# Kernel optimization log

Hardware: AMD Instinct MI355X
Metric: run time of the kernel (lower is better)

## Reference

```python
import jax, jax.numpy as jnp
import numpy as np

RNN_HID = 256
WINDOW = 128
SEQ_LEN = 8192
BATCH = 32
NEG_INF = -1e9


def setup_inputs() -> dict:
    key = jax.random.key(0)
    k1, k2, k3, k4, k5 = jax.random.split(key, 5)
    h_t = jax.random.normal(k1, (BATCH, RNN_HID), dtype=jnp.float32)
    encoder_outputs = jax.random.normal(k2, (BATCH, SEQ_LEN, RNN_HID), dtype=jnp.float32)
    # learned parameters (torch nn.Linear default init approximated with scaled normals)
    W_p = jax.random.normal(k3, (RNN_HID, RNN_HID), dtype=jnp.float32) / jnp.sqrt(RNN_HID)
    v_p = jax.random.normal(k4, (RNN_HID,), dtype=jnp.float32)
    w_att = jax.random.normal(k5, (RNN_HID,), dtype=jnp.float32) / jnp.sqrt(RNN_HID)
    return {"h_t": h_t, "encoder_outputs": encoder_outputs, "W_p": W_p, "v_p": v_p, "w_att": w_att}


def reference(h_t, encoder_outputs, W_p, v_p, w_att):
    B, S, H = encoder_outputs.shape
    # predicted center position p_t per sample
    tanh_out = jnp.tanh(h_t @ W_p.T)                      # [B, H]
    p_t = SEQ_LEN * jax.nn.sigmoid(tanh_out @ v_p)        # [B]
    p_t = jnp.clip(jnp.round(p_t).astype(jnp.int32), 0, SEQ_LEN - 1)
    start = jnp.maximum(p_t - WINDOW, 0)                  # [B]
    end = jnp.minimum(p_t + WINDOW, SEQ_LEN)              # [B]
    rng = jnp.arange(S)[None, :]                          # [1, S]
    mask = (rng >= start[:, None]) & (rng < end[:, None])  # [B, S]
    # scores on masked (zeroed) encoder outputs, then masked softmax
    local = encoder_outputs * mask[:, :, None].astype(encoder_outputs.dtype)
    scores = jnp.einsum('bsh,h->bs', local, w_att)        # [B, S]
    scores = jnp.where(mask, scores, NEG_INF)
    attn_weights = jax.nn.softmax(scores, axis=-1)        # [B, S]
    context_vector = jnp.einsum('bs,bsh->bh', attn_weights, encoder_outputs)
    return context_vector, attn_weights
```

## Files before the change

### kernel.cpp

```cpp
#include <hip/hip_runtime.h>
#include <math.h>

#define BATCH   32
#define SEQ     8192
#define HID     256
#define WIN     128
#define NSLICE  8
#define SLROWS  32

#define WS_PT_OFF   0
#define WS_EXP_OFF  1024
#define WS_SUM_OFF  33792
#define WS_CTX_OFF  34816

__global__ __launch_bounds__(256) void k1_pt_partials(
    const float* __restrict__ h_t,
    const float* __restrict__ W_p,
    const float* __restrict__ v_p,
    float* __restrict__ attn_out,
    double* __restrict__ ws_pt)
{
    const int blk = blockIdx.x;
    const int b   = blk >> 2;
    const int q   = blk & 3;
    const int tid = threadIdx.x;

    __shared__ float  hs[HID];
    __shared__ double part[256];
    __shared__ double redv[64];

    hs[tid] = h_t[b * HID + tid];

    {
        float4* az = (float4*)attn_out + (size_t)blk * 512;
        float4 z = make_float4(0.f, 0.f, 0.f, 0.f);
        az[tid]       = z;
        az[tid + 256] = z;
    }
    __syncthreads();

    const int jl = tid >> 2;
    const int j  = q * 64 + jl;
    const int p4 = tid & 3;
    const float4* wrow = (const float4*)(W_p + (size_t)j * HID + p4 * 64);
    const float*  h4   = &hs[p4 * 64];
    double acc = 0.0;
#pragma unroll
    for (int k = 0; k < 16; ++k) {
        float4 w = wrow[k];
        acc += (double)w.x * h4[k*4+0] + (double)w.y * h4[k*4+1]
             + (double)w.z * h4[k*4+2] + (double)w.w * h4[k*4+3];
    }
    part[tid] = acc;
    __syncthreads();

    if (p4 == 0) {
        double s = part[tid] + part[tid+1] + part[tid+2] + part[tid+3];
        float  t = tanhf((float)s);
        redv[jl] = (double)t * (double)v_p[j];
    }
    __syncthreads();
    for (int off = 32; off > 0; off >>= 1) {
        if (tid < off) redv[tid] += redv[tid + off];
        __syncthreads();
    }
    if (tid == 0) ws_pt[b * 4 + q] = redv[0];
}

__device__ __forceinline__ void window_from_partials(const double* ws_pt, int b,
                                                     int* start, int* end) {
    double x = ws_pt[b*4+0] + ws_pt[b*4+1] + ws_pt[b*4+2] + ws_pt[b*4+3];
    float xf = (float)x;
    float sg = 1.0f / (1.0f + expf(-xf));
    float p  = (float)SEQ * sg;
    int pr = (int)rintf(p);
    pr = min(max(pr, 0), SEQ - 1);
    *start = max(pr - WIN, 0);
    *end   = min(pr + WIN, SEQ);
}

__global__ __launch_bounds__(256) void k2_scores_ctx(
    const float* __restrict__ enc,
    const float* __restrict__ w_att,
    const double* __restrict__ ws_pt,
    float* __restrict__ ws_exp,
    float* __restrict__ ws_sum,
    float* __restrict__ ws_ctx)
{
    const int blk = blockIdx.x;
    const int b   = blk >> 3;
    const int s   = blk & 7;
    const int tid = threadIdx.x;

    __shared__ float wa[HID];
    __shared__ float partial[256];
    __shared__ float es[SLROWS];
    __shared__ int   win_s[2];

    wa[tid] = w_att[tid];
    if (tid == 0) {
        int st, en;
        window_from_partials(ws_pt, b, &st, &en);
        win_s[0] = st; win_s[1] = en;
    }
    __syncthreads();

    const int start = win_s[0];
    const int end   = win_s[1];
    const int g0    = start + s * SLROWS;

    {
        const int r   = tid >> 3;
        const int seg = tid & 7;
        const int g   = g0 + r;
        const int gc  = (g < end) ? g : start;
        const float4* rowp = (const float4*)(enc + ((size_t)b * SEQ + gc) * HID + seg * 32);
        const float*  w4   = &wa[seg * 32];
        float sc = 0.f;
#pragma unroll
        for (int k = 0; k < 8; ++k) {
            float4 e = rowp[k];
            sc += e.x * w4[k*4+0] + e.y * w4[k*4+1] + e.z * w4[k*4+2] + e.w * w4[k*4+3];
        }
        partial[tid] = sc;
    }
    __syncthreads();

    if (tid < SLROWS) {
        const int base = tid * 8;
        float scr = 0.f;
#pragma unroll
        for (int k = 0; k < 8; ++k) scr += partial[base + k];
        const int g = g0 + tid;
        float ev = (g < end) ? expf(scr) : 0.f;
        es[tid] = ev;
        ws_exp[b * 256 + s * SLROWS + tid] = ev;
    }
    __syncthreads();

    if (tid == 0) {
        float sm = 0.f;
#pragma unroll
        for (int k = 0; k < SLROWS; ++k) sm += es[k];
        ws_sum[b * NSLICE + s] = sm;
    }

    {
        float acc = 0.f;
        if (g0 + SLROWS - 1 < end) {
            const float* basep = enc + ((size_t)b * SEQ + g0) * HID + tid;
#pragma unroll
            for (int i = 0; i < SLROWS; ++i)
                acc += es[i] * basep[(size_t)i * HID];
        } else {
#pragma unroll
            for (int i = 0; i < SLROWS; ++i) {
                int g  = g0 + i;
                int gc = (g < end) ? g : start;
                acc += es[i] * enc[((size_t)b * SEQ + gc) * HID + tid];
            }
        }
        ws_ctx[((size_t)b * NSLICE + s) * HID + tid] = acc;
    }
}

__global__ __launch_bounds__(256) void k3_finalize(
    const double* __restrict__ ws_pt,
    const float* __restrict__ ws_exp,
    const float* __restrict__ ws_sum,
    const float* __restrict__ ws_ctx,
    float* __restrict__ ctx_out,
    float* __restrict__ attn_out)
{
    const int b   = blockIdx.x;
    const int tid = threadIdx.x;

    __shared__ int   win_s[2];
    __shared__ float inv_s;

    if (tid == 0) {
        int st, en;
        window_from_partials(ws_pt, b, &st, &en);
        win_s[0] = st; win_s[1] = en;
        float dsum = 0.f;
#pragma unroll
        for (int k = 0; k < NSLICE; ++k) dsum += ws_sum[b * NSLICE + k];
        inv_s = 1.0f / dsum;
    }
    __syncthreads();

    const int start = win_s[0];
    const int L     = win_s[1] - win_s[0];
    const float inv = inv_s;

    float acc = 0.f;
#pragma unroll
    for (int s = 0; s < NSLICE; ++s)
        acc += ws_ctx[((size_t)b * NSLICE + s) * HID + tid];
    ctx_out[b * HID + tid] = acc * inv;

    if (tid < L)
        attn_out[(size_t)b * SEQ + start + tid] = ws_exp[b * 256 + tid] * inv;
}

extern "C" void kernel_launch(void* const* d_in, const int* in_sizes, int n_in,
                              void* d_out, int out_size, void* d_ws, size_t ws_size,
                              hipStream_t stream) {
    const float* h_t   = (const float*)d_in[0];
    const float* enc   = (const float*)d_in[1];
    const float* W_p   = (const float*)d_in[2];
    const float* v_p   = (const float*)d_in[3];
    const float* w_att = (const float*)d_in[4];

    float* ctx_out  = (float*)d_out;
    float* attn_out = (float*)d_out + BATCH * HID;

    char* ws = (char*)d_ws;
    double* ws_pt  = (double*)(ws + WS_PT_OFF);
    float*  ws_exp = (float*)(ws + WS_EXP_OFF);
    float*  ws_sum = (float*)(ws + WS_SUM_OFF);
    float*  ws_ctx = (float*)(ws + WS_CTX_OFF);

    k1_pt_partials<<<BATCH * 4, 256, 0, stream>>>(h_t, W_p, v_p, attn_out, ws_pt);
    k2_scores_ctx<<<BATCH * NSLICE, 256, 0, stream>>>(enc, w_att, ws_pt, ws_exp, ws_sum, ws_ctx);
    k3_finalize<<<BATCH, 256, 0, stream>>>(ws_pt, ws_exp, ws_sum, ws_ctx, ctx_out, attn_out);
}
```

Measured before the change: 15.88 us.

## Fuse position prediction, scoring and finalize into one kernel with last-block reduction

Merges the three kernels into a single launch. Each slice block recomputes the full W_p matvec, tanh and v_p reduction for its batch row to get the window. The last block to finish for each batch, detected with an atomic counter and thread fences, then performs the final normalisation and writes the outputs. This removes two kernel launches and their inter-kernel gaps, but adds an 8x redundant 256x256 fp64 matvec per batch row with poorly coalesced row-per-thread reads of W_p, plus a memset to reset the counters.

After: 49.05 us. 3.09x slower.

```diff
diff --git a/kernel.cpp b/kernel.cpp
--- a/kernel.cpp
+++ b/kernel.cpp
@@ -5,103 +5,77 @@
 #define SEQ     8192
 #define HID     256
 #define WIN     128
-#define NSLICE  8
+#define NSL     8
 #define SLROWS  32
 
-#define WS_PT_OFF   0
-#define WS_EXP_OFF  1024
-#define WS_SUM_OFF  33792
+#define WS_EXP_OFF  0
+#define WS_SUM_OFF  32768
+#define WS_CNT_OFF  33792
 #define WS_CTX_OFF  34816
 
-__global__ __launch_bounds__(256) void k1_pt_partials(
+__global__ __launch_bounds__(256) void fused_local_attn(
     const float* __restrict__ h_t,
+    const float* __restrict__ enc,
     const float* __restrict__ W_p,
     const float* __restrict__ v_p,
+    const float* __restrict__ w_att,
+    float* __restrict__ ctx_out,
     float* __restrict__ attn_out,
-    double* __restrict__ ws_pt)
-{
-    const int blk = blockIdx.x;
-    const int b   = blk >> 2;
-    const int q   = blk & 3;
-    const int tid = threadIdx.x;
-
-    __shared__ float  hs[HID];
-    __shared__ double part[256];
-    __shared__ double redv[64];
-
-    hs[tid] = h_t[b * HID + tid];
-
-    {
-        float4* az = (float4*)attn_out + (size_t)blk * 512;
-        float4 z = make_float4(0.f, 0.f, 0.f, 0.f);
-        az[tid]       = z;
-        az[tid + 256] = z;
-    }
-    __syncthreads();
-
-    const int jl = tid >> 2;
-    const int j  = q * 64 + jl;
-    const int p4 = tid & 3;
-    const float4* wrow = (const float4*)(W_p + (size_t)j * HID + p4 * 64);
-    const float*  h4   = &hs[p4 * 64];
-    double acc = 0.0;
-#pragma unroll
-    for (int k = 0; k < 16; ++k) {
-        float4 w = wrow[k];
-        acc += (double)w.x * h4[k*4+0] + (double)w.y * h4[k*4+1]
-             + (double)w.z * h4[k*4+2] + (double)w.w * h4[k*4+3];
-    }
-    part[tid] = acc;
-    __syncthreads();
-
-    if (p4 == 0) {
-        double s = part[tid] + part[tid+1] + part[tid+2] + part[tid+3];
-        float  t = tanhf((float)s);
-        redv[jl] = (double)t * (double)v_p[j];
-    }
-    __syncthreads();
-    for (int off = 32; off > 0; off >>= 1) {
-        if (tid < off) redv[tid] += redv[tid + off];
-        __syncthreads();
-    }
-    if (tid == 0) ws_pt[b * 4 + q] = redv[0];
-}
-
-__device__ __forceinline__ void window_from_partials(const double* ws_pt, int b,
-                                                     int* start, int* end) {
-    double x = ws_pt[b*4+0] + ws_pt[b*4+1] + ws_pt[b*4+2] + ws_pt[b*4+3];
-    float xf = (float)x;
-    float sg = 1.0f / (1.0f + expf(-xf));
-    float p  = (float)SEQ * sg;
-    int pr = (int)rintf(p);
-    pr = min(max(pr, 0), SEQ - 1);
-    *start = max(pr - WIN, 0);
-    *end   = min(pr + WIN, SEQ);
-}
-
-__global__ __launch_bounds__(256) void k2_scores_ctx(
-    const float* __restrict__ enc,
-    const float* __restrict__ w_att,
-    const double* __restrict__ ws_pt,
     float* __restrict__ ws_exp,
     float* __restrict__ ws_sum,
-    float* __restrict__ ws_ctx)
+    float* __restrict__ ws_ctx,
+    int*   __restrict__ counters)
 {
     const int blk = blockIdx.x;
     const int b   = blk >> 3;
     const int s   = blk & 7;
     const int tid = threadIdx.x;
 
-    __shared__ float wa[HID];
-    __shared__ float partial[256];
-    __shared__ float es[SLROWS];
-    __shared__ int   win_s[2];
+    __shared__ float  hs[HID];
+    __shared__ float  wa[HID];
+    __shared__ double wred[4];
+    __shared__ float  partial[256];
+    __shared__ float  es[SLROWS];
+    __shared__ int    win_s[2];
+    __shared__ int    is_last;
+    __shared__ float  inv_s;
 
+    hs[tid] = h_t[b * HID + tid];
     wa[tid] = w_att[tid];
+
+    {
+        float4* az = (float4*)(attn_out + (size_t)b * SEQ + (size_t)s * 1024);
+        az[tid] = make_float4(0.f, 0.f, 0.f, 0.f);
+    }
+    __syncthreads();
+
+    {
+        const float4* wrow = (const float4*)(W_p + (size_t)tid * HID);
+        double a0 = 0.0, a1 = 0.0, a2 = 0.0, a3 = 0.0;
+#pragma unroll 4
+        for (int k = 0; k < 64; k += 4) {
+            float4 w0 = wrow[k], w1 = wrow[k+1], w2 = wrow[k+2], w3 = wrow[k+3];
+            const float* h4 = &hs[4 * k];
+            a0 += (double)w0.x*h4[0]  + (double)w0.y*h4[1]  + (double)w0.z*h4[2]  + (double)w0.w*h4[3];
+            a1 += (double)w1.x*h4[4]  + (double)w1.y*h4[5]  + (double)w1.z*h4[6]  + (double)w1.w*h4[7];
+            a2 += (double)w2.x*h4[8]  + (double)w2.y*h4[9]  + (double)w2.z*h4[10] + (double)w2.w*h4[11];
+            a3 += (double)w3.x*h4[12] + (double)w3.y*h4[13] + (double)w3.z*h4[14] + (double)w3.w*h4[15];
+        }
+        float  t   = tanhf((float)(a0 + a1 + a2 + a3));
+        double val = (double)t * (double)v_p[tid];
+        for (int off = 32; off > 0; off >>= 1) val += __shfl_down(val, off, 64);
+        if ((tid & 63) == 0) wred[tid >> 6] = val;
+    }
+    __syncthreads();
     if (tid == 0) {
-        int st, en;
-        window_from_partials(ws_pt, b, &st, &en);
-        win_s[0] = st; win_s[1] = en;
+        double x  = wred[0] + wred[1] + wred[2] + wred[3];
+        float  xf = (float)x;
+        float  sg = 1.0f / (1.0f + expf(-xf));
+        float  p  = (float)SEQ * sg;
+        int pr = (int)rintf(p);
+        pr = min(max(pr, 0), SEQ - 1);
+        win_s[0] = max(pr - WIN, 0);
+        win_s[1] = min(pr + WIN, SEQ);
     }
     __syncthreads();
 
@@ -142,7 +116,7 @@
         float sm = 0.f;
 #pragma unroll
         for (int k = 0; k < SLROWS; ++k) sm += es[k];
-        ws_sum[b * NSLICE + s] = sm;
+        ws_sum[b * NSL + s] = sm;
     }
 
     {
@@ -160,45 +134,32 @@
                 acc += es[i] * enc[((size_t)b * SEQ + gc) * HID + tid];
             }
         }
-        ws_ctx[((size_t)b * NSLICE + s) * HID + tid] = acc;
+        ws_ctx[((size_t)b * NSL + s) * HID + tid] = acc;
     }
-}
 
-__global__ __launch_bounds__(256) void k3_finalize(
-    const double* __restrict__ ws_pt,
-    const float* __restrict__ ws_exp,
-    const float* __restrict__ ws_sum,
-    const float* __restrict__ ws_ctx,
-    float* __restrict__ ctx_out,
-    float* __restrict__ attn_out)
-{
-    const int b   = blockIdx.x;
-    const int tid = threadIdx.x;
-
-    __shared__ int   win_s[2];
-    __shared__ float inv_s;
+    __threadfence();
+    __syncthreads();
+    if (tid == 0) is_last = (atomicAdd(&counters[b], 1) == NSL - 1);
+    __syncthreads();
+    if (!is_last) return;
+    __threadfence();
 
     if (tid == 0) {
-        int st, en;
-        window_from_partials(ws_pt, b, &st, &en);
-        win_s[0] = st; win_s[1] = en;
         float dsum = 0.f;
 #pragma unroll
-        for (int k = 0; k < NSLICE; ++k) dsum += ws_sum[b * NSLICE + k];
+        for (int k = 0; k < NSL; ++k) dsum += ws_sum[b * NSL + k];
         inv_s = 1.0f / dsum;
     }
     __syncthreads();
 
-    const int start = win_s[0];
-    const int L     = win_s[1] - win_s[0];
     const float inv = inv_s;
-
     float acc = 0.f;
 #pragma unroll
-    for (int s = 0; s < NSLICE; ++s)
-        acc += ws_ctx[((size_t)b * NSLICE + s) * HID + tid];
+    for (int k = 0; k < NSL; ++k)
+        acc += ws_ctx[((size_t)b * NSL + k) * HID + tid];
     ctx_out[b * HID + tid] = acc * inv;
 
+    const int L = end - start;
     if (tid < L)
         attn_out[(size_t)b * SEQ + start + tid] = ws_exp[b * 256 + tid] * inv;
 }
@@ -215,13 +176,14 @@
     float* ctx_out  = (float*)d_out;
     float* attn_out = (float*)d_out + BATCH * HID;
 
-    char* ws = (char*)d_ws;
-    double* ws_pt  = (double*)(ws + WS_PT_OFF);
-    float*  ws_exp = (float*)(ws + WS_EXP_OFF);
-    float*  ws_sum = (float*)(ws + WS_SUM_OFF);
-    float*  ws_ctx = (float*)(ws + WS_CTX_OFF);
+    char*  ws       = (char*)d_ws;
+    float* ws_exp   = (float*)(ws + WS_EXP_OFF);
+    float* ws_sum   = (float*)(ws + WS_SUM_OFF);
+    int*   counters = (int*)  (ws + WS_CNT_OFF);
+    float* ws_ctx   = (float*)(ws + WS_CTX_OFF);
 
-    k1_pt_partials<<<BATCH * 4, 256, 0, stream>>>(h_t, W_p, v_p, attn_out, ws_pt);
-    k2_scores_ctx<<<BATCH * NSLICE, 256, 0, stream>>>(enc, w_att, ws_pt, ws_exp, ws_sum, ws_ctx);
-    k3_finalize<<<BATCH, 256, 0, stream>>>(ws_pt, ws_exp, ws_sum, ws_ctx, ctx_out, attn_out);
+    hipMemsetAsync(counters, 0, BATCH * sizeof(int), stream);
+    fused_local_attn<<<BATCH * NSL, 256, 0, stream>>>(
+        h_t, enc, W_p, v_p, w_att, ctx_out, attn_out,
+        ws_exp, ws_sum, ws_ctx, counters);
 }
```

## Stage encoder rows in LDS for context reuse and split p_t projection wider

Applied to the files above, without the earlier changes.

The scores kernel now copies each 32-row encoder slice into a padded shared-memory tile while computing scores, then builds the context partial from that tile instead of reading the same rows from global memory a second time. The p_t kernel is split into 8 blocks per batch instead of 4, with a warp-shuffle reduction replacing the shared-memory tree and each block zeroing a smaller part of the attention output. This cuts global traffic and adds parallelism to the first stage, at the cost of about 33KB of LDS per block in the scores kernel, which may lower occupancy.

Result: no change. 16.11 us (+1.4%).

```diff
diff --git a/kernel.cpp b/kernel.cpp
--- a/kernel.cpp
+++ b/kernel.cpp
@@ -5,15 +5,17 @@
 #define SEQ     8192
 #define HID     256
 #define WIN     128
-#define NSLICE  8
+#define NSL     8
 #define SLROWS  32
+#define NQ      8
+#define TPAD    260
 
 #define WS_PT_OFF   0
-#define WS_EXP_OFF  1024
-#define WS_SUM_OFF  33792
-#define WS_CTX_OFF  34816
-
-__global__ __launch_bounds__(256) void k1_pt_partials(
+#define WS_EXP_OFF  2048
+#define WS_SUM_OFF  34816
+#define WS_CTX_OFF  35840
+
+__global__ __launch_bounds__(256) void k1_pt(
     const float* __restrict__ h_t,
     const float* __restrict__ W_p,
     const float* __restrict__ v_p,
@@ -21,55 +23,50 @@
     double* __restrict__ ws_pt)
 {
     const int blk = blockIdx.x;
-    const int b   = blk >> 2;
-    const int q   = blk & 3;
+    const int b   = blk >> 3;
+    const int q   = blk & 7;
     const int tid = threadIdx.x;
 
     __shared__ float  hs[HID];
-    __shared__ double part[256];
-    __shared__ double redv[64];
+    __shared__ double red[256];
 
     hs[tid] = h_t[b * HID + tid];
 
-    {
-        float4* az = (float4*)attn_out + (size_t)blk * 512;
-        float4 z = make_float4(0.f, 0.f, 0.f, 0.f);
-        az[tid]       = z;
-        az[tid + 256] = z;
-    }
-    __syncthreads();
-
-    const int jl = tid >> 2;
-    const int j  = q * 64 + jl;
-    const int p4 = tid & 3;
-    const float4* wrow = (const float4*)(W_p + (size_t)j * HID + p4 * 64);
-    const float*  h4   = &hs[p4 * 64];
+    ((float4*)attn_out)[(size_t)blk * 256 + tid] = make_float4(0.f, 0.f, 0.f, 0.f);
+    __syncthreads();
+
+    const int jl = tid >> 3;
+    const int j  = q * 32 + jl;
+    const int ks = tid & 7;
+    const float4* wrow = (const float4*)(W_p + (size_t)j * HID + ks * 32);
+    const float*  h4   = &hs[ks * 32];
     double acc = 0.0;
 #pragma unroll
-    for (int k = 0; k < 16; ++k) {
+    for (int k = 0; k < 8; ++k) {
         float4 w = wrow[k];
         acc += (double)w.x * h4[k*4+0] + (double)w.y * h4[k*4+1]
              + (double)w.z * h4[k*4+2] + (double)w.w * h4[k*4+3];
     }
-    part[tid] = acc;
-    __syncthreads();
-
-    if (p4 == 0) {
-        double s = part[tid] + part[tid+1] + part[tid+2] + part[tid+3];
-        float  t = tanhf((float)s);
-        redv[jl] = (double)t * (double)v_p[j];
-    }
-    __syncthreads();
-    for (int off = 32; off > 0; off >>= 1) {
-        if (tid < off) redv[tid] += redv[tid + off];
-        __syncthreads();
-    }
-    if (tid == 0) ws_pt[b * 4 + q] = redv[0];
+    red[tid] = acc;
+    __syncthreads();
+
+    if (tid < 32) {
+        double s = 0.0;
+#pragma unroll
+        for (int k = 0; k < 8; ++k) s += red[tid * 8 + k];
+        float  t   = tanhf((float)s);
+        double val = (double)t * (double)v_p[q * 32 + tid];
+        for (int off = 16; off > 0; off >>= 1)
+            val += __shfl_down(val, off, 32);
+        if (tid == 0) ws_pt[b * NQ + q] = val;
+    }
 }
 
 __device__ __forceinline__ void window_from_partials(const double* ws_pt, int b,
                                                      int* start, int* end) {
-    double x = ws_pt[b*4+0] + ws_pt[b*4+1] + ws_pt[b*4+2] + ws_pt[b*4+3];
+    double x = 0.0;
+#pragma unroll
+    for (int k = 0; k < NQ; ++k) x += ws_pt[b * NQ + k];
     float xf = (float)x;
     float sg = 1.0f / (1.0f + expf(-xf));
     float p  = (float)SEQ * sg;
@@ -92,16 +89,27 @@
     const int s   = blk & 7;
     const int tid = threadIdx.x;
 
-    __shared__ float wa[HID];
-    __shared__ float partial[256];
-    __shared__ float es[SLROWS];
-    __shared__ int   win_s[2];
+    __shared__ float  wa[HID];
+    __shared__ float  tile[SLROWS][TPAD];
+    __shared__ float  partial[256];
+    __shared__ float  es[SLROWS];
+    __shared__ double redd[NQ];
+    __shared__ int    win_s[2];
 
     wa[tid] = w_att[tid];
+    if (tid < NQ) redd[tid] = ws_pt[b * NQ + tid];
+    __syncthreads();
     if (tid == 0) {
-        int st, en;
-        window_from_partials(ws_pt, b, &st, &en);
-        win_s[0] = st; win_s[1] = en;
+        double x = 0.0;
+#pragma unroll
+        for (int k = 0; k < NQ; ++k) x += redd[k];
+        float xf = (float)x;
+        float sg = 1.0f / (1.0f + expf(-xf));
+        float p  = (float)SEQ * sg;
+        int pr = (int)rintf(p);
+        pr = min(max(pr, 0), SEQ - 1);
+        win_s[0] = max(pr - WIN, 0);
+        win_s[1] = min(pr + WIN, SEQ);
     }
     __syncthreads();
 
@@ -110,16 +118,18 @@
     const int g0    = start + s * SLROWS;
 
     {
-        const int r   = tid >> 3;
-        const int seg = tid & 7;
-        const int g   = g0 + r;
-        const int gc  = (g < end) ? g : start;
-        const float4* rowp = (const float4*)(enc + ((size_t)b * SEQ + gc) * HID + seg * 32);
-        const float*  w4   = &wa[seg * 32];
+        const int r  = tid >> 3;
+        const int ks = tid & 7;
+        const int g  = g0 + r;
+        const int gc = (g < end) ? g : start;
+        const float4* rowp = (const float4*)(enc + ((size_t)b * SEQ + gc) * HID + ks * 32);
+        const float*  w4   = &wa[ks * 32];
+        float4* trow = (float4*)&tile[r][ks * 32];
         float sc = 0.f;
 #pragma unroll
         for (int k = 0; k < 8; ++k) {
             float4 e = rowp[k];
+            trow[k] = e;
             sc += e.x * w4[k*4+0] + e.y * w4[k*4+1] + e.z * w4[k*4+2] + e.w * w4[k*4+3];
         }
         partial[tid] = sc;
@@ -127,10 +137,9 @@
     __syncthreads();
 
     if (tid < SLROWS) {
-        const int base = tid * 8;
         float scr = 0.f;
 #pragma unroll
-        for (int k = 0; k < 8; ++k) scr += partial[base + k];
+        for (int k = 0; k < 8; ++k) scr += partial[tid * 8 + k];
         const int g = g0 + tid;
         float ev = (g < end) ? expf(scr) : 0.f;
         es[tid] = ev;
@@ -142,25 +151,15 @@
         float sm = 0.f;
 #pragma unroll
         for (int k = 0; k < SLROWS; ++k) sm += es[k];
-        ws_sum[b * NSLICE + s] = sm;
+        ws_sum[b * NSL + s] = sm;
     }
 
     {
         float acc = 0.f;
-        if (g0 + SLROWS - 1 < end) {
-            const float* basep = enc + ((size_t)b * SEQ + g0) * HID + tid;
-#pragma unroll
-            for (int i = 0; i < SLROWS; ++i)
-                acc += es[i] * basep[(size_t)i * HID];
-        } else {
-#pragma unroll
-            for (int i = 0; i < SLROWS; ++i) {
-                int g  = g0 + i;
-                int gc = (g < end) ? g : start;
-                acc += es[i] * enc[((size_t)b * SEQ + gc) * HID + tid];
-            }
-        }
-        ws_ctx[((size_t)b * NSLICE + s) * HID + tid] = acc;
+#pragma unroll
+        for (int i = 0; i < SLROWS; ++i)
+            acc += es[i] * tile[i][tid];
+        ws_ctx[((size_t)b * NSL + s) * HID + tid] = acc;
     }
 }
 
@@ -184,21 +183,20 @@
         win_s[0] = st; win_s[1] = en;
         float dsum = 0.f;
 #pragma unroll
-        for (int k = 0; k < NSLICE; ++k) dsum += ws_sum[b * NSLICE + k];
+        for (int k = 0; k < NSL; ++k) dsum += ws_sum[b * NSL + k];
         inv_s = 1.0f / dsum;
     }
     __syncthreads();
+
+    const float inv = inv_s;
+    float acc = 0.f;
+#pragma unroll
+    for (int k = 0; k < NSL; ++k)
+        acc += ws_ctx[((size_t)b * NSL + k) * HID + tid];
+    ctx_out[b * HID + tid] = acc * inv;
 
     const int start = win_s[0];
     const int L     = win_s[1] - win_s[0];
-    const float inv = inv_s;
-
-    float acc = 0.f;
-#pragma unroll
-    for (int s = 0; s < NSLICE; ++s)
-        acc += ws_ctx[((size_t)b * NSLICE + s) * HID + tid];
-    ctx_out[b * HID + tid] = acc * inv;
-
     if (tid < L)
         attn_out[(size_t)b * SEQ + start + tid] = ws_exp[b * 256 + tid] * inv;
 }
@@ -215,13 +213,13 @@
     float* ctx_out  = (float*)d_out;
     float* attn_out = (float*)d_out + BATCH * HID;
 
-    char* ws = (char*)d_ws;
+    char*   ws     = (char*)d_ws;
     double* ws_pt  = (double*)(ws + WS_PT_OFF);
-    float*  ws_exp = (float*)(ws + WS_EXP_OFF);
-    float*  ws_sum = (float*)(ws + WS_SUM_OFF);
-    float*  ws_ctx = (float*)(ws + WS_CTX_OFF);
-
-    k1_pt_partials<<<BATCH * 4, 256, 0, stream>>>(h_t, W_p, v_p, attn_out, ws_pt);
-    k2_scores_ctx<<<BATCH * NSLICE, 256, 0, stream>>>(enc, w_att, ws_pt, ws_exp, ws_sum, ws_ctx);
+    float*  ws_exp = (float*) (ws + WS_EXP_OFF);
+    float*  ws_sum = (float*) (ws + WS_SUM_OFF);
+    float*  ws_ctx = (float*) (ws + WS_CTX_OFF);
+
+    k1_pt<<<BATCH * NQ, 256, 0, stream>>>(h_t, W_p, v_p, attn_out, ws_pt);
+    k2_scores_ctx<<<BATCH * NSL, 256, 0, stream>>>(enc, w_att, ws_pt, ws_exp, ws_sum, ws_ctx);
     k3_finalize<<<BATCH, 256, 0, stream>>>(ws_pt, ws_exp, ws_sum, ws_ctx, ctx_out, attn_out);
 }
```
